# Performance work log

Measured on AMD Instinct MI355X. Metric: run time of the kernel, lower is better.

The kernel has to match this reference:

```python
import jax, jax.numpy as jnp
import numpy as np

N_BLADES = 8
GRADE = np.array([0, 1, 1, 1, 2, 2, 2, 3])
WEIGHT_EXPANSION = np.array([0, 1, 1, 1, 2, 2, 2, 3])
GRADE_BLADES = ([0], [1, 2, 3], [4, 5, 6], [7])
EPS = 1e-6


def _build_cayley():
    # Blades as bitmasks over generators e1,e2,e3; canonical order = sorted by (grade, mask)
    # -> [1, e1, e2, e3, e12, e13, e23, e123], matching weight_expansion [0,1,1,1,2,2,2,3].
    masks = sorted(range(8), key=lambda m: (bin(m).count('1'), m))
    m2i = {m: i for i, m in enumerate(masks)}
    ti, tj, tk, ts, triples = [], [], [], [], []
    for i, a in enumerate(masks):
        for j, b in enumerate(masks):
            # reorder sign for Euclidean Cl(3,0): count transpositions
            swaps = sum(bin(a >> (bit + 1)).count('1') for bit in range(3) if (b >> bit) & 1)
            k = m2i[a ^ b]
            ti.append(i); tj.append(j); tk.append(k)
            ts.append(-1.0 if swaps % 2 else 1.0)
            triples.append((int(GRADE[i]), int(GRADE[j]), int(GRADE[k])))
    uniq = sorted(set(triples))  # 20 directed grade-interaction paths for P3M0
    pidx = {t: p for p, t in enumerate(uniq)}
    tp = np.array([pidx[t] for t in triples])
    return (np.array(ti), np.array(tj), np.array(tk),
            np.array(ts, dtype=np.float32), tp, len(uniq))


TI, TJ, TK, TS, TP, NUM_PATHS = _build_cayley()  # NUM_PATHS == 20


def _forward(x, linear_weight, linear_bias, gp_weight, normalize=True):
    # grade-wise linear map via blade-expanded weights: y[k] = x[k] @ W[grade(k)] + b
    y = jnp.einsum('kbi,kio->kbo', x, linear_weight[WEIGHT_EXPANSION]) + linear_bias
    y = jax.nn.gelu(y, approximate=True)
    # steerable weighted geometric product: one learnable weight per feature per grade path
    wpath = gp_weight.T[TP]  # [64, F]: path weight for each blade-product term
    terms = (TS[:, None, None] * wpath[:, None, :]) * x[TI] * y[TJ]  # [64, B, F]
    out = jax.ops.segment_sum(terms, TK, num_segments=N_BLADES)  # [8, B, F]
    if normalize:
        # grade-wise RMS norm: per sample, normalize each grade subspace over its blades and features
        parts = []
        for blades in GRADE_BLADES:
            og = out[np.array(blades)]  # [n_blades_g, B, F]
            rms = jnp.sqrt(jnp.mean(og * og, axis=(0, 2), keepdims=True) + EPS)
            parts.append(og / rms)
        out = jnp.concatenate(parts, axis=0)
    return out


def setup_inputs() -> dict:
    key = jax.random.key(0)
    k1, k2, k3 = jax.random.split(key, 3)
    B, F = 4096, 512
    x = jax.random.normal(k1, (N_BLADES, B, F), dtype=jnp.float32)
    gp_weight = jax.random.normal(k2, (F, NUM_PATHS), dtype=jnp.float32) * np.float32(1.0 / np.sqrt(3 + 1))
    linear_weight = jax.random.normal(k3, (4, F, F), dtype=jnp.float32) * np.float32(1.0 / np.sqrt(F))
    linear_bias = jnp.zeros((1, 1, F), dtype=jnp.float32)
    return {"x": x, "linear_weight": linear_weight, "linear_bias": linear_bias, "gp_weight": gp_weight}


def reference(x, linear_weight, linear_bias, gp_weight):
    return _forward(x, linear_weight, linear_bias, gp_weight, normalize=True)
```

## Files before the change

kernel.cpp:

```cpp
#include <hip/hip_runtime.h>

typedef short short8v __attribute__((ext_vector_type(8)));
typedef float f32x4 __attribute__((ext_vector_type(4)));
typedef unsigned short u16;
typedef unsigned int u32;

__device__ __forceinline__ u16 f2bf(float f) {
    u32 u = __float_as_uint(f);
    u += 0x7FFFu + ((u >> 16) & 1u);
    return (u16)(u >> 16);
}
__device__ __forceinline__ float bf2f(u16 h) {
    return __uint_as_float(((u32)h) << 16);
}
__device__ __forceinline__ float gelu_f(float v) {
    float u = 0.7978845608028654f * fmaf(0.044715f * v, v * v, v);
    return 0.5f * v * (1.0f + tanhf(u));
}

__global__ __launch_bounds__(256) void k_prep(const float* __restrict__ x, u16* __restrict__ xpk,
                                              const float* __restrict__ w, u16* __restrict__ wpk) {
    const int bid = blockIdx.x, tid = threadIdx.x;
    if (bid < 8192) {
        int t = bid * 256 + tid;
        int lane = t & 63, kb = (t >> 6) & 15, r16 = t >> 10;
        int row = r16 * 16 + (lane & 15);
        int k0 = kb * 32 + (lane >> 4) * 8;
        const float4* src = (const float4*)(x + (size_t)row * 512 + k0);
        float4 a = src[0], c = src[1];
        short8v s;
        s[0] = (short)f2bf(a.x); s[1] = (short)f2bf(a.y); s[2] = (short)f2bf(a.z); s[3] = (short)f2bf(a.w);
        s[4] = (short)f2bf(c.x); s[5] = (short)f2bf(c.y); s[6] = (short)f2bf(c.z); s[7] = (short)f2bf(c.w);
        *(short8v*)(xpk + (size_t)t * 8) = s;
    } else {
        int t = (bid - 8192) * 256 + tid;
        int lane = t & 63, kb = (t >> 6) & 15, c16 = (t >> 10) & 31, g = t >> 15;
        int col = c16 * 16 + (lane & 15);
        int k0 = kb * 32 + (lane >> 4) * 8;
        const float* src = w + (size_t)g * 262144 + (size_t)k0 * 512 + col;
        short8v s;
#pragma unroll
        for (int j = 0; j < 8; j++) s[j] = (short)f2bf(src[(size_t)j * 512]);
        *(short8v*)(wpk + (size_t)t * 8) = s;
    }
}

__global__ __launch_bounds__(256) void k_gemm(const u16* __restrict__ xpk, const u16* __restrict__ wpk,
                                              const float* __restrict__ bias, u16* __restrict__ yb) {
    const int tid = threadIdx.x;
    const int w = tid >> 6, lane = tid & 63;
    const int bid = blockIdx.x;
    const int mt = bid >> 2, nt = bid & 3;
    const int WE[8] = {0, 1, 1, 1, 2, 2, 2, 3};
    const int g = WE[mt >> 5];
    const int wr = w >> 1, wc = w & 1;
    const int loff = lane * 16;

    const char* Ab = (const char*)xpk + (size_t)(mt * 8 + wr * 4) * 16384 + loff;
    const char* Bb = (const char*)wpk + (size_t)(g * 32 + nt * 8 + wc * 4) * 16384 + loff;

    f32x4 acc[4][4];
#pragma unroll
    for (int m = 0; m < 4; m++)
#pragma unroll
        for (int n = 0; n < 4; n++) acc[m][n] = (f32x4){0.f, 0.f, 0.f, 0.f};

    short8v a0[4], b0[4], a1[4], b1[4];

#define LOADF(AR, BR, KB) { \
    _Pragma("unroll") \
    for (int m = 0; m < 4; m++) AR[m] = *(const short8v*)(Ab + (size_t)m * 16384 + (KB) * 1024); \
    _Pragma("unroll") \
    for (int n = 0; n < 4; n++) BR[n] = *(const short8v*)(Bb + (size_t)n * 16384 + (KB) * 1024); \
    }
#define MM(AR, BR) { \
    _Pragma("unroll") \
    for (int m = 0; m < 4; m++) \
        _Pragma("unroll") \
        for (int n = 0; n < 4; n++) \
            acc[m][n] = __builtin_amdgcn_mfma_f32_16x16x32_bf16(AR[m], BR[n], acc[m][n], 0, 0, 0); \
    }

    LOADF(a0, b0, 0);
#pragma unroll
    for (int kb = 0; kb < 14; kb += 2) {
        LOADF(a1, b1, kb + 1);
        MM(a0, b0);
        LOADF(a0, b0, kb + 2);
        MM(a1, b1);
    }
    LOADF(a1, b1, 15);
    MM(a0, b0);
    MM(a1, b1);
#undef LOADF
#undef MM

    const size_t row0 = (size_t)mt * 128 + wr * 64;
    const int colBase = nt * 128 + wc * 64;
#pragma unroll
    for (int n = 0; n < 4; n++) {
        int col = colBase + n * 16 + (lane & 15);
        float bv = bias[col];
#pragma unroll
        for (int m = 0; m < 4; m++) {
#pragma unroll
            for (int j = 0; j < 4; j++) {
                size_t row = row0 + m * 16 + (lane >> 4) * 4 + j;
                float v = acc[m][n][j] + bv;
                yb[row * 512 + col] = f2bf(gelu_f(v));
            }
        }
    }
}

#define TERM(i, j, k, s, p) o[ff][k] = fmaf(s * wp[ff][p], xv[ff][i] * yv[ff][j], o[ff][k]);
#define GP_ALL \
    TERM(0,0,0, 1.0f,0) TERM(0,1,1, 1.0f,1) TERM(0,2,2, 1.0f,1) TERM(0,3,3, 1.0f,1) \
    TERM(0,4,4, 1.0f,2) TERM(0,5,5, 1.0f,2) TERM(0,6,6, 1.0f,2) TERM(0,7,7, 1.0f,3) \
    TERM(1,0,1, 1.0f,4) TERM(1,1,0, 1.0f,5) TERM(1,2,4, 1.0f,6) TERM(1,3,5, 1.0f,6) \
    TERM(1,4,2, 1.0f,7) TERM(1,5,3, 1.0f,7) TERM(1,6,7, 1.0f,8) TERM(1,7,6, 1.0f,9) \
    TERM(2,0,2, 1.0f,4) TERM(2,1,4,-1.0f,6) TERM(2,2,0, 1.0f,5) TERM(2,3,6, 1.0f,6) \
    TERM(2,4,1,-1.0f,7) TERM(2,5,7,-1.0f,8) TERM(2,6,3, 1.0f,7) TERM(2,7,5,-1.0f,9) \
    TERM(3,0,3, 1.0f,4) TERM(3,1,5,-1.0f,6) TERM(3,2,6,-1.0f,6) TERM(3,3,0, 1.0f,5) \
    TERM(3,4,7, 1.0f,8) TERM(3,5,1,-1.0f,7) TERM(3,6,2,-1.0f,7) TERM(3,7,4, 1.0f,9) \
    TERM(4,0,4, 1.0f,10) TERM(4,1,2,-1.0f,11) TERM(4,2,1, 1.0f,11) TERM(4,3,7, 1.0f,12) \
    TERM(4,4,0,-1.0f,13) TERM(4,5,6,-1.0f,14) TERM(4,6,5, 1.0f,14) TERM(4,7,3,-1.0f,15) \
    TERM(5,0,5, 1.0f,10) TERM(5,1,3,-1.0f,11) TERM(5,2,7,-1.0f,12) TERM(5,3,1, 1.0f,11) \
    TERM(5,4,6, 1.0f,14) TERM(5,5,0,-1.0f,13) TERM(5,6,4,-1.0f,14) TERM(5,7,2, 1.0f,15) \
    TERM(6,0,6, 1.0f,10) TERM(6,1,7, 1.0f,12) TERM(6,2,3,-1.0f,11) TERM(6,3,2, 1.0f,11) \
    TERM(6,4,5,-1.0f,14) TERM(6,5,4, 1.0f,14) TERM(6,6,0,-1.0f,13) TERM(6,7,1,-1.0f,15) \
    TERM(7,0,7, 1.0f,16) TERM(7,1,6, 1.0f,17) TERM(7,2,5,-1.0f,17) TERM(7,3,4, 1.0f,17) \
    TERM(7,4,3,-1.0f,18) TERM(7,5,2, 1.0f,18) TERM(7,6,1,-1.0f,18) TERM(7,7,0,-1.0f,19)

__global__ __launch_bounds__(256) void k_gp(const float* __restrict__ x, const u16* __restrict__ yb,
                                            const float* __restrict__ gp, float* __restrict__ out) {
    const int b = blockIdx.x, tid = threadIdx.x;
    const int w = tid >> 6, lane = tid & 63;
    const int f0 = tid * 2;

    float xv[2][8], yv[2][8], wp[2][20], o[2][8];
#pragma unroll
    for (int i = 0; i < 8; i++) {
        float2 xf = *(const float2*)(x + ((size_t)i * 4096 + b) * 512 + f0);
        xv[0][i] = xf.x; xv[1][i] = xf.y;
        u32 uy = *(const u32*)(yb + ((size_t)i * 4096 + b) * 512 + f0);
        yv[0][i] = bf2f((u16)(uy & 0xFFFF)); yv[1][i] = bf2f((u16)(uy >> 16));
    }
#pragma unroll
    for (int ff = 0; ff < 2; ++ff) {
        const float4* gv = (const float4*)(gp + (size_t)(f0 + ff) * 20);
#pragma unroll
        for (int q = 0; q < 5; ++q) {
            float4 v = gv[q];
            wp[ff][q * 4 + 0] = v.x; wp[ff][q * 4 + 1] = v.y;
            wp[ff][q * 4 + 2] = v.z; wp[ff][q * 4 + 3] = v.w;
        }
    }

    float ss[4] = {0.f, 0.f, 0.f, 0.f};
#pragma unroll
    for (int ff = 0; ff < 2; ++ff) {
#pragma unroll
        for (int k = 0; k < 8; k++) o[ff][k] = 0.f;
        GP_ALL
        ss[0] += o[ff][0] * o[ff][0];
        ss[1] += o[ff][1] * o[ff][1] + o[ff][2] * o[ff][2] + o[ff][3] * o[ff][3];
        ss[2] += o[ff][4] * o[ff][4] + o[ff][5] * o[ff][5] + o[ff][6] * o[ff][6];
        ss[3] += o[ff][7] * o[ff][7];
    }

#pragma unroll
    for (int g2 = 0; g2 < 4; g2++) {
        float v = ss[g2];
#pragma unroll
        for (int off = 32; off >= 1; off >>= 1) v += __shfl_xor(v, off);
        ss[g2] = v;
    }
    __shared__ float red[4][4];
    if (lane == 0) { red[w][0] = ss[0]; red[w][1] = ss[1]; red[w][2] = ss[2]; red[w][3] = ss[3]; }
    __syncthreads();
    float inv[4];
    const float cnt[4] = {512.f, 1536.f, 1536.f, 512.f};
#pragma unroll
    for (int g2 = 0; g2 < 4; g2++) {
        float tot = red[0][g2] + red[1][g2] + red[2][g2] + red[3][g2];
        inv[g2] = 1.0f / sqrtf(tot / cnt[g2] + 1e-6f);
    }
    const int GK[8] = {0, 1, 1, 1, 2, 2, 2, 3};
#pragma unroll
    for (int k = 0; k < 8; k++) {
        float2 st;
        st.x = o[0][k] * inv[GK[k]];
        st.y = o[1][k] * inv[GK[k]];
        *(float2*)(out + ((size_t)k * 4096 + b) * 512 + f0) = st;
    }
}

extern "C" void kernel_launch(void* const* d_in, const int* in_sizes, int n_in,
                              void* d_out, int out_size, void* d_ws, size_t ws_size,
                              hipStream_t stream) {
    const float* x  = (const float*)d_in[0];
    const float* lw = (const float*)d_in[1];
    const float* lb = (const float*)d_in[2];
    const float* gp = (const float*)d_in[3];
    float* out = (float*)d_out;
    char* ws = (char*)d_ws;
    u16* xpk = (u16*)ws;
    u16* wpk = (u16*)(ws + 33554432);
    u16* yb  = (u16*)(ws + 35651584);

    hipLaunchKernelGGL(k_prep, dim3(8704), dim3(256), 0, stream, x, xpk, lw, wpk);
    hipLaunchKernelGGL(k_gemm, dim3(1024), dim3(256), 0, stream, xpk, wpk, lb, yb);
    hipLaunchKernelGGL(k_gp, dim3(4096), dim3(256), 0, stream, x, yb, gp, out);
}
```

Measured before the change: 196.8 us.

## Fuse x bf16 conversion into GEMM, move GELU to GP kernel, swizzle blocks

```diff
diff --git a/kernel.cpp b/kernel.cpp
--- a/kernel.cpp
+++ b/kernel.cpp
@@ -13,51 +13,47 @@
 __device__ __forceinline__ float bf2f(u16 h) {
     return __uint_as_float(((u32)h) << 16);
 }
-__device__ __forceinline__ float gelu_f(float v) {
+__device__ __forceinline__ u32 cvtpk(float a, float b) {
+    u32 d;
+    asm("v_cvt_pk_bf16_f32 %0, %1, %2" : "=v"(d) : "v"(a), "v"(b));
+    return d;
+}
+__device__ __forceinline__ short8v pack8(float4 a, float4 b) {
+    union { u32 u[4]; short8v s; } r;
+    r.u[0] = cvtpk(a.x, a.y); r.u[1] = cvtpk(a.z, a.w);
+    r.u[2] = cvtpk(b.x, b.y); r.u[3] = cvtpk(b.z, b.w);
+    return r.s;
+}
+__device__ __forceinline__ float gelu_sig(float v) {
     float u = 0.7978845608028654f * fmaf(0.044715f * v, v * v, v);
-    return 0.5f * v * (1.0f + tanhf(u));
-}
-
-__global__ __launch_bounds__(256) void k_prep(const float* __restrict__ x, u16* __restrict__ xpk,
-                                              const float* __restrict__ w, u16* __restrict__ wpk) {
-    const int bid = blockIdx.x, tid = threadIdx.x;
-    if (bid < 8192) {
-        int t = bid * 256 + tid;
-        int lane = t & 63, kb = (t >> 6) & 15, r16 = t >> 10;
-        int row = r16 * 16 + (lane & 15);
-        int k0 = kb * 32 + (lane >> 4) * 8;
-        const float4* src = (const float4*)(x + (size_t)row * 512 + k0);
-        float4 a = src[0], c = src[1];
-        short8v s;
-        s[0] = (short)f2bf(a.x); s[1] = (short)f2bf(a.y); s[2] = (short)f2bf(a.z); s[3] = (short)f2bf(a.w);
-        s[4] = (short)f2bf(c.x); s[5] = (short)f2bf(c.y); s[6] = (short)f2bf(c.z); s[7] = (short)f2bf(c.w);
-        *(short8v*)(xpk + (size_t)t * 8) = s;
-    } else {
-        int t = (bid - 8192) * 256 + tid;
-        int lane = t & 63, kb = (t >> 6) & 15, c16 = (t >> 10) & 31, g = t >> 15;
-        int col = c16 * 16 + (lane & 15);
-        int k0 = kb * 32 + (lane >> 4) * 8;
-        const float* src = w + (size_t)g * 262144 + (size_t)k0 * 512 + col;
-        short8v s;
-#pragma unroll
-        for (int j = 0; j < 8; j++) s[j] = (short)f2bf(src[(size_t)j * 512]);
-        *(short8v*)(wpk + (size_t)t * 8) = s;
-    }
-}
-
-__global__ __launch_bounds__(256) void k_gemm(const u16* __restrict__ xpk, const u16* __restrict__ wpk,
+    return v / (1.0f + __expf(-2.0f * u));
+}
+
+__global__ __launch_bounds__(256) void k_prep(const float* __restrict__ w, u16* __restrict__ wpk) {
+    int t = blockIdx.x * 256 + threadIdx.x;
+    int lane = t & 63, kb = (t >> 6) & 15, c16 = (t >> 10) & 31, g = t >> 15;
+    int col = c16 * 16 + (lane & 15);
+    int k0 = kb * 32 + (lane >> 4) * 8;
+    const float* src = w + (size_t)g * 262144 + (size_t)k0 * 512 + col;
+    short8v s;
+#pragma unroll
+    for (int j = 0; j < 8; j++) s[j] = (short)f2bf(src[(size_t)j * 512]);
+    *(short8v*)(wpk + (size_t)t * 8) = s;
+}
+
+__global__ __launch_bounds__(256) void k_gemm(const float* __restrict__ x, const u16* __restrict__ wpk,
                                               const float* __restrict__ bias, u16* __restrict__ yb) {
     const int tid = threadIdx.x;
     const int w = tid >> 6, lane = tid & 63;
     const int bid = blockIdx.x;
-    const int mt = bid >> 2, nt = bid & 3;
+    const int swz = (bid & 7) * 128 + (bid >> 3);
+    const int mt = swz >> 2, nt = swz & 3;
     const int WE[8] = {0, 1, 1, 1, 2, 2, 2, 3};
     const int g = WE[mt >> 5];
     const int wr = w >> 1, wc = w & 1;
-    const int loff = lane * 16;
-
-    const char* Ab = (const char*)xpk + (size_t)(mt * 8 + wr * 4) * 16384 + loff;
-    const char* Bb = (const char*)wpk + (size_t)(g * 32 + nt * 8 + wc * 4) * 16384 + loff;
+
+    const float* Af = x + ((size_t)(mt * 128 + wr * 64 + (lane & 15))) * 512 + (lane >> 4) * 8;
+    const char* Bb = (const char*)wpk + (size_t)(g * 32 + nt * 8 + wc * 4) * 16384 + lane * 16;
 
     f32x4 acc[4][4];
 #pragma unroll
@@ -65,35 +61,44 @@
 #pragma unroll
         for (int n = 0; n < 4; n++) acc[m][n] = (f32x4){0.f, 0.f, 0.f, 0.f};
 
-    short8v a0[4], b0[4], a1[4], b1[4];
-
-#define LOADF(AR, BR, KB) { \
-    _Pragma("unroll") \
-    for (int m = 0; m < 4; m++) AR[m] = *(const short8v*)(Ab + (size_t)m * 16384 + (KB) * 1024); \
+    float4 fa0[4][2], fa1[4][2];
+    short8v b0[4], b1[4];
+
+#define LOADA(FA, KB) { \
+    _Pragma("unroll") \
+    for (int m = 0; m < 4; m++) { \
+        const float4* p = (const float4*)(Af + (size_t)m * 8192 + (KB) * 32); \
+        FA[m][0] = p[0]; FA[m][1] = p[1]; \
+    } }
+#define LOADB(BR, KB) { \
     _Pragma("unroll") \
     for (int n = 0; n < 4; n++) BR[n] = *(const short8v*)(Bb + (size_t)n * 16384 + (KB) * 1024); \
     }
-#define MM(AR, BR) { \
+#define MMA(FA, BR) { \
+    short8v af[4]; \
+    _Pragma("unroll") \
+    for (int m = 0; m < 4; m++) af[m] = pack8(FA[m][0], FA[m][1]); \
     _Pragma("unroll") \
     for (int m = 0; m < 4; m++) \
         _Pragma("unroll") \
         for (int n = 0; n < 4; n++) \
-            acc[m][n] = __builtin_amdgcn_mfma_f32_16x16x32_bf16(AR[m], BR[n], acc[m][n], 0, 0, 0); \
-    }
-
-    LOADF(a0, b0, 0);
+            acc[m][n] = __builtin_amdgcn_mfma_f32_16x16x32_bf16(af[m], BR[n], acc[m][n], 0, 0, 0); \
+    }
+
+    LOADA(fa0, 0); LOADB(b0, 0);
 #pragma unroll
     for (int kb = 0; kb < 14; kb += 2) {
-        LOADF(a1, b1, kb + 1);
-        MM(a0, b0);
-        LOADF(a0, b0, kb + 2);
-        MM(a1, b1);
-    }
-    LOADF(a1, b1, 15);
-    MM(a0, b0);
-    MM(a1, b1);
-#undef LOADF
-#undef MM
+        LOADA(fa1, kb + 1); LOADB(b1, kb + 1);
+        MMA(fa0, b0);
+        LOADA(fa0, kb + 2); LOADB(b0, kb + 2);
+        MMA(fa1, b1);
+    }
+    LOADA(fa1, 15); LOADB(b1, 15);
+    MMA(fa0, b0);
+    MMA(fa1, b1);
+#undef LOADA
+#undef LOADB
+#undef MMA
 
     const size_t row0 = (size_t)mt * 128 + wr * 64;
     const int colBase = nt * 128 + wc * 64;
@@ -106,8 +111,7 @@
 #pragma unroll
             for (int j = 0; j < 4; j++) {
                 size_t row = row0 + m * 16 + (lane >> 4) * 4 + j;
-                float v = acc[m][n][j] + bv;
-                yb[row * 512 + col] = f2bf(gelu_f(v));
+                yb[row * 512 + col] = f2bf(acc[m][n][j] + bv);
             }
         }
     }
@@ -144,7 +148,8 @@
         float2 xf = *(const float2*)(x + ((size_t)i * 4096 + b) * 512 + f0);
         xv[0][i] = xf.x; xv[1][i] = xf.y;
         u32 uy = *(const u32*)(yb + ((size_t)i * 4096 + b) * 512 + f0);
-        yv[0][i] = bf2f((u16)(uy & 0xFFFF)); yv[1][i] = bf2f((u16)(uy >> 16));
+        yv[0][i] = gelu_sig(bf2f((u16)(uy & 0xFFFF)));
+        yv[1][i] = gelu_sig(bf2f((u16)(uy >> 16)));
     }
 #pragma unroll
     for (int ff = 0; ff < 2; ++ff) {
@@ -205,11 +210,10 @@
     const float* gp = (const float*)d_in[3];
     float* out = (float*)d_out;
     char* ws = (char*)d_ws;
-    u16* xpk = (u16*)ws;
-    u16* wpk = (u16*)(ws + 33554432);
-    u16* yb  = (u16*)(ws + 35651584);
-
-    hipLaunchKernelGGL(k_prep, dim3(8704), dim3(256), 0, stream, x, xpk, lw, wpk);
-    hipLaunchKernelGGL(k_gemm, dim3(1024), dim3(256), 0, stream, xpk, wpk, lb, yb);
+    u16* wpk = (u16*)ws;
+    u16* yb  = (u16*)(ws + 2097152);
+
+    hipLaunchKernelGGL(k_prep, dim3(512), dim3(256), 0, stream, lw, wpk);
+    hipLaunchKernelGGL(k_gemm, dim3(1024), dim3(256), 0, stream, x, wpk, lb, yb);
     hipLaunchKernelGGL(k_gp, dim3(4096), dim3(256), 0, stream, x, yb, gp, out);
 }
```

Measured after the change: 213.9 us. +8.7%, slower.
